# Kernel optimization log

Measured on AMD Instinct MI355X. Metric: run time of the kernel, lower is better.

## Reference

```python
import jax, jax.numpy as jnp
import numpy as np


def setup_inputs() -> dict:
    key = jax.random.key(0)
    k1, k2 = jax.random.split(key)
    B, T, V = 128, 256, 256
    batch = jax.random.normal(k1, (B, T, V, 3), dtype=jnp.float32)
    missing = jax.random.uniform(k2, (B, T, V)) < 0.2
    labels = jnp.where(missing, -1.0, 1.0)
    batch = batch.at[..., 0].set(labels)
    return {"batch": batch}


def reference(batch):
    B, T, V, _ = batch.shape
    dt = batch.dtype
    # constant-velocity model matrices (hardcoded in the module)
    F = jnp.array([[1, 0, 1, 0], [0, 1, 0, 1], [0, 0, 1, 0], [0, 0, 0, 1]], dtype=dt)
    H = jnp.array([[1, 0, 0, 0], [0, 1, 0, 0]], dtype=dt)
    Q = jnp.eye(4, dtype=dt) * 0.01
    R = jnp.eye(2, dtype=dt) * 1.0
    I4 = jnp.eye(4, dtype=dt)

    s0 = jnp.zeros((B, V, 4), dtype=dt)
    P0 = jnp.broadcast_to(jnp.eye(4, dtype=dt) * 1000.0, (B, V, 4, 4))

    obs_t = jnp.moveaxis(batch, 1, 0)  # (T, B, V, 3)

    def step(carry, obs):
        s, P = carry  # s: (B,V,4), P: (B,V,4,4)
        labels = obs[..., 0]
        z = obs[..., 1:]                       # (B,V,2)
        mask = (labels != -1)[..., None]       # (B,V,1)
        s_pred = jnp.einsum('bvj,ij->bvi', s, F)                 # s @ F.T
        P_pred = jnp.einsum('ij,bvjk,lk->bvil', F, P, F) + Q     # F P F^T + Q
        y = (z - s_pred[..., :2]) * mask                          # (B,V,2)
        S = P_pred[..., :2, :2] + R                               # H P H^T + R
        K = jnp.einsum('bvij,bvjk->bvik', P_pred[..., :, :2], jnp.linalg.inv(S))  # (B,V,4,2)
        s_upd = s_pred + jnp.einsum('bvij,bvj->bvi', K, y) * mask
        KH = jnp.einsum('bvij,jk->bvik', K, H)                    # (B,V,4,4)
        P_upd = jnp.einsum('bvij,bvjk->bvik', I4 - KH, P_pred)
        s_new = jnp.where(mask, s_upd, s_pred)
        P_new = jnp.where(mask[..., None], P_upd, P_pred)
        return (s_new, P_new), None

    (s_final, _), _ = jax.lax.scan(step, (s0, P0), obs_t)
    last_pos = s_final[..., :2]                                   # (B,V,2)
    ones = jnp.ones((B, V, 1), dtype=dt)
    return jnp.concatenate((ones, last_pos), axis=-1)             # (B,V,3)
```

## Files before the change

### kernel.cpp

```cpp
#include <hip/hip_runtime.h>
#include <stdint.h>


#define KF_B 128
#define KF_T 256
#define KF_V 256
#define KF_C 16
#define KF_L 16
#define KF_W 16
#define KF_NT (KF_B * KF_V)
#define KF_NG (KF_NT / 64)

typedef float f2 __attribute__((ext_vector_type(2)));

#define KF_PK(label)                                                    \
    const float q00 = p00 + 2.f * p01 + p11 + 0.01f;                    \
    const float q01 = p01 + p11;                                        \
    const float q11 = p11 + 0.01f;                                      \
    const float S = q00 + 1.f;                                          \
    const float m = ((label) != -1.0f) ? 1.0f : 0.0f;                   \
    const float is = m * __builtin_amdgcn_rcpf(S);                      \
    const float K0 = q00 * is;                                          \
    const float K1 = q01 * is;                                          \
    p00 = q00 - K0 * q00;                                               \
    p01 = q01 - K0 * q01;                                               \
    p11 = q11 - K1 * q01;

__global__ __launch_bounds__(64, 8) void kf_scan(const float* __restrict__ batch,
                                                 float* __restrict__ ws) {
    const int blk = blockIdx.x;
    const int chunk = blk >> 9;
    const int g = blk & (KF_NG - 1);
    const int track = g * 64 + threadIdx.x;
    const int b = track >> 8;
    const int v = track & (KF_V - 1);

    const int stride = KF_V * 3;
    const float* __restrict__ base =
        batch + ((size_t)b * KF_T * KF_V + v) * 3;

    float p00 = 1000.f, p01 = 0.f, p11 = 1000.f;

    const float* p;
    if (chunk != 0) {
        p = base + (size_t)(KF_L * (chunk - 1)) * stride;
#pragma unroll 4
        for (int t = 0; t < KF_W; ++t) {
            const float label = p[0];
            p += stride;
            KF_PK(label);
        }
    } else {
        p = base;
    }

    f2 mA = {1.f, 0.f};
    f2 mB = {0.f, 1.f};
    f2 dp = {0.f, 0.f};
    f2 dv = {0.f, 0.f};

#pragma unroll 4
    for (int t = 0; t < KF_L; ++t) {
        const float label = p[0];
        const f2 z = {p[1], p[2]};
        p += stride;
        KF_PK(label);
        const float a = 1.f - K0;
        const f2 tm = mA + mB;
        mA = a * tm;
        mB = mB - K1 * tm;
        const f2 s = dp + dv;
        dp = a * s + K0 * z;
        dv = dv + K1 * (z - s);
    }

    float* w = ws + ((size_t)chunk * KF_NT + track) * 8;
    *(float4*)(w)     = make_float4(mA.x, mA.y, mB.x, mB.y);
    *(float4*)(w + 4) = make_float4(dp.x, dp.y, dv.x, dv.y);
}

__global__ __launch_bounds__(64) void kf_compose(const float* __restrict__ ws,
                                                 float* __restrict__ out) {
    const int track = blockIdx.x * 64 + threadIdx.x;
    f2 x = {0.f, 0.f};
    f2 v = {0.f, 0.f};
#pragma unroll
    for (int c = 0; c < KF_C; ++c) {
        const float* w = ws + ((size_t)c * KF_NT + track) * 8;
        const float4 a = *(const float4*)(w);
        const float4 d = *(const float4*)(w + 4);
        const f2 dpv = {d.x, d.y};
        const f2 dvv = {d.z, d.w};
        const f2 nx = a.x * x + a.y * v + dpv;
        const f2 nv = a.z * x + a.w * v + dvv;
        x = nx; v = nv;
    }
    float* o = out + (size_t)track * 3;
    o[0] = 1.0f;
    o[1] = x.x;
    o[2] = x.y;
}

extern "C" void kernel_launch(void* const* d_in, const int* in_sizes, int n_in,
                              void* d_out, int out_size, void* d_ws, size_t ws_size,
                              hipStream_t stream) {
    (void)in_sizes; (void)n_in; (void)ws_size; (void)out_size;
    const float* batch = (const float*)d_in[0];
    float* out = (float*)d_out;
    float* ws = (float*)d_ws;

    kf_scan<<<KF_C * KF_NG, 64, 0, stream>>>(batch, ws);
    kf_compose<<<KF_NG, 64, 0, stream>>>(ws, out);
}
```

Before: 155.8 us.

## Fuse chunked scan and compose into one kernel using LDS label sharing

Merges the two-kernel chunked Kalman scan into one kernel. Each 1024-thread block handles 64 tracks, with one wave per time chunk. Each wave loads its chunk's labels into LDS so the next wave can run its covariance warm-up without re-reading global memory. Per-chunk affine maps are composed through LDS instead of a global workspace. This removes the second launch, the workspace round-trip and the duplicate label loads, at the cost of 64 KB of LDS per block, block-wide barriers and a serial compose done by one wave while the other 15 wait.

```diff
diff --git a/kernel.cpp b/kernel.cpp
--- a/kernel.cpp
+++ b/kernel.cpp
@@ -7,7 +7,6 @@
 #define KF_V 256
 #define KF_C 16
 #define KF_L 16
-#define KF_W 16
 #define KF_NT (KF_B * KF_V)
 #define KF_NG (KF_NT / 64)
 
@@ -26,89 +25,94 @@
     p01 = q01 - K0 * q01;                                               \
     p11 = q11 - K1 * q01;
 
-__global__ __launch_bounds__(64, 8) void kf_scan(const float* __restrict__ batch,
-                                                 float* __restrict__ ws) {
-    const int blk = blockIdx.x;
-    const int chunk = blk >> 9;
-    const int g = blk & (KF_NG - 1);
-    const int track = g * 64 + threadIdx.x;
+__global__ __launch_bounds__(1024, 4) void kf_fused(const float* __restrict__ batch,
+                                                    float* __restrict__ out) {
+    __shared__ float lds[KF_C * KF_L * 64];
+
+    const int lane = threadIdx.x & 63;
+    const int w    = threadIdx.x >> 6;
+    const int track = blockIdx.x * 64 + lane;
     const int b = track >> 8;
     const int v = track & (KF_V - 1);
 
     const int stride = KF_V * 3;
     const float* __restrict__ base =
         batch + ((size_t)b * KF_T * KF_V + v) * 3;
+    const float* __restrict__ pc = base + (size_t)(w * KF_L) * stride;
+
+    float lab[KF_L];
+    f2 z[KF_L];
+#pragma unroll
+    for (int t = 0; t < KF_L; ++t) {
+        const float* q = pc + t * stride;
+        lab[t] = q[0];
+        z[t].x = q[1];
+        z[t].y = q[2];
+        lds[(w * KF_L + t) * 64 + lane] = lab[t];
+    }
+    __syncthreads();
 
     float p00 = 1000.f, p01 = 0.f, p11 = 1000.f;
 
-    const float* p;
-    if (chunk != 0) {
-        p = base + (size_t)(KF_L * (chunk - 1)) * stride;
-#pragma unroll 4
-        for (int t = 0; t < KF_W; ++t) {
-            const float label = p[0];
-            p += stride;
+    if (w != 0) {
+#pragma unroll
+        for (int t = 0; t < KF_L; ++t) {
+            const float label = lds[((w - 1) * KF_L + t) * 64 + lane];
             KF_PK(label);
         }
-    } else {
-        p = base;
     }
 
     f2 mA = {1.f, 0.f};
     f2 mB = {0.f, 1.f};
     f2 dp = {0.f, 0.f};
     f2 dv = {0.f, 0.f};
-
-#pragma unroll 4
+#pragma unroll
     for (int t = 0; t < KF_L; ++t) {
-        const float label = p[0];
-        const f2 z = {p[1], p[2]};
-        p += stride;
+        const float label = lab[t];
+        const f2 zz = z[t];
         KF_PK(label);
         const float a = 1.f - K0;
         const f2 tm = mA + mB;
         mA = a * tm;
         mB = mB - K1 * tm;
         const f2 s = dp + dv;
-        dp = a * s + K0 * z;
-        dv = dv + K1 * (z - s);
+        dp = a * s + K0 * zz;
+        dv = dv + K1 * (zz - s);
     }
 
-    float* w = ws + ((size_t)chunk * KF_NT + track) * 8;
-    *(float4*)(w)     = make_float4(mA.x, mA.y, mB.x, mB.y);
-    *(float4*)(w + 4) = make_float4(dp.x, dp.y, dv.x, dv.y);
-}
+    __syncthreads();
+    {
+        float* mp = &lds[(w * 64 + lane) * 9];
+        mp[0] = mA.x; mp[1] = mA.y; mp[2] = mB.x; mp[3] = mB.y;
+        mp[4] = dp.x; mp[5] = dp.y; mp[6] = dv.x; mp[7] = dv.y;
+    }
+    __syncthreads();
 
-__global__ __launch_bounds__(64) void kf_compose(const float* __restrict__ ws,
-                                                 float* __restrict__ out) {
-    const int track = blockIdx.x * 64 + threadIdx.x;
-    f2 x = {0.f, 0.f};
-    f2 v = {0.f, 0.f};
+    if (w == 0) {
+        f2 x = {0.f, 0.f};
+        f2 vv = {0.f, 0.f};
 #pragma unroll
-    for (int c = 0; c < KF_C; ++c) {
-        const float* w = ws + ((size_t)c * KF_NT + track) * 8;
-        const float4 a = *(const float4*)(w);
-        const float4 d = *(const float4*)(w + 4);
-        const f2 dpv = {d.x, d.y};
-        const f2 dvv = {d.z, d.w};
-        const f2 nx = a.x * x + a.y * v + dpv;
-        const f2 nv = a.z * x + a.w * v + dvv;
-        x = nx; v = nv;
+        for (int c = 0; c < KF_C; ++c) {
+            const float* q = &lds[(c * 64 + lane) * 9];
+            const float a00 = q[0], a01 = q[1], a10 = q[2], a11 = q[3];
+            const f2 dpp = {q[4], q[5]};
+            const f2 dvv = {q[6], q[7]};
+            const f2 nx = a00 * x + a01 * vv + dpp;
+            const f2 nv = a10 * x + a11 * vv + dvv;
+            x = nx; vv = nv;
+        }
+        float* o = out + (size_t)track * 3;
+        o[0] = 1.0f;
+        o[1] = x.x;
+        o[2] = x.y;
     }
-    float* o = out + (size_t)track * 3;
-    o[0] = 1.0f;
-    o[1] = x.x;
-    o[2] = x.y;
 }
 
 extern "C" void kernel_launch(void* const* d_in, const int* in_sizes, int n_in,
                               void* d_out, int out_size, void* d_ws, size_t ws_size,
                               hipStream_t stream) {
-    (void)in_sizes; (void)n_in; (void)ws_size; (void)out_size;
+    (void)in_sizes; (void)n_in; (void)d_ws; (void)ws_size; (void)out_size;
     const float* batch = (const float*)d_in[0];
     float* out = (float*)d_out;
-    float* ws = (float*)d_ws;
-
-    kf_scan<<<KF_C * KF_NG, 64, 0, stream>>>(batch, ws);
-    kf_compose<<<KF_NG, 64, 0, stream>>>(ws, out);
+    kf_fused<<<KF_NG, 1024, 0, stream>>>(batch, out);
 }
```

New measurement: 153.7 us. About the same (-1.3%).
